# Performance work log

Hardware: AMD Instinct MI355X
Metric: run time of the kernel (lower is better)

## Reference

```python
import jax, jax.numpy as jnp
import numpy as np

D_IN = 2048
D_OUT = 2048
NUM_HEADS = 32
NUM_KV_GROUPS = 8
HEAD_DIM = D_OUT // NUM_HEADS          # 64
GROUP_SIZE = NUM_HEADS // NUM_KV_GROUPS  # 4
BATCH = 2
SEQ = 2048


def _rope(x, cos, sin):
    # x: [b, h, s, d]; cos/sin: [s, d]
    d = x.shape[-1]
    x1, x2 = x[..., : d // 2], x[..., d // 2:]
    rotated = jnp.concatenate((-x2, x1), axis=-1)
    return x * cos[None, None, :, :] + rotated * sin[None, None, :, :]


def setup_inputs() -> dict:
    key = jax.random.key(0)
    ks = jax.random.split(key, 8)
    x = jax.random.normal(ks[0], (BATCH, SEQ, D_IN), dtype=jnp.float32)
    cos = jax.random.normal(ks[1], (SEQ, HEAD_DIM), dtype=jnp.float32)
    sin = jax.random.normal(ks[2], (SEQ, HEAD_DIM), dtype=jnp.float32)
    # causal mask: True above the diagonal = masked out
    mask = jnp.triu(jnp.ones((SEQ, SEQ), dtype=jnp.bool_), k=1)
    s = 0.02
    Wq = jax.random.normal(ks[3], (D_IN, D_OUT), dtype=jnp.float32) * s
    Wk = jax.random.normal(ks[4], (D_IN, NUM_KV_GROUPS * HEAD_DIM), dtype=jnp.float32) * s
    Wv = jax.random.normal(ks[5], (D_IN, NUM_KV_GROUPS * HEAD_DIM), dtype=jnp.float32) * s
    Wo = jax.random.normal(ks[6], (D_OUT, D_OUT), dtype=jnp.float32) * s
    return {"x": x, "cos": cos, "sin": sin, "mask": mask,
            "Wq": Wq, "Wk": Wk, "Wv": Wv, "Wo": Wo}


def reference(x, cos, sin, mask, Wq, Wk, Wv, Wo):
    b, s, _ = x.shape
    # projections (Linear, no bias): weights stored as [d_in, d_out]
    q = (x @ Wq).reshape(b, s, NUM_HEADS, HEAD_DIM).transpose(0, 2, 1, 3)      # [b,H,s,d]
    k = (x @ Wk).reshape(b, s, NUM_KV_GROUPS, HEAD_DIM).transpose(0, 2, 1, 3)  # [b,G,s,d]
    v = (x @ Wv).reshape(b, s, NUM_KV_GROUPS, HEAD_DIM).transpose(0, 2, 1, 3)  # [b,G,s,d]
    q = _rope(q, cos, sin)
    k = _rope(k, cos, sin)
    # GQA broadcast: repeat each KV group group_size times along head axis
    k = jnp.repeat(k, GROUP_SIZE, axis=1)  # [b,H,s,d]
    v = jnp.repeat(v, GROUP_SIZE, axis=1)  # [b,H,s,d]
    scores = jnp.einsum('bhqd,bhkd->bhqk', q, k)
    scores = jnp.where(mask[None, None, :, :], -jnp.inf, scores)
    # original scales AFTER masking: softmax(scores / sqrt(head_dim)); -inf stays -inf
    attn = jax.nn.softmax(scores * (1.0 / np.sqrt(HEAD_DIM)), axis=-1)
    ctx = jnp.einsum('bhqk,bhkd->bqhd', attn, v).reshape(b, s, D_OUT)
    return ctx @ Wo
```

## Files before the change

### kernel.cpp

```cpp
#include <hip/hip_runtime.h>
#include <hip/hip_fp16.h>

#define SEQ    2048
#define DIN    2048
#define DOUT   2048
#define NH     32
#define NKV    8
#define HD     64
#define BB     2

typedef _Float16 half_t;
typedef __attribute__((ext_vector_type(8))) _Float16 half8;
typedef __attribute__((ext_vector_type(4))) _Float16 half4;
typedef __attribute__((ext_vector_type(2))) __fp16   fp16x2;
typedef __attribute__((ext_vector_type(4))) float    floatx4;

union H8U { half8 h; int u[4]; };
union H2I { fp16x2 h; int i; };

__device__ __forceinline__ void gload16(void* l, const void* g) {
    __builtin_amdgcn_global_load_lds(
        (const __attribute__((address_space(1))) void*)g,
        (__attribute__((address_space(3))) void*)l, 16, 0, 0);
}

__global__ void cast_f2h(const float* __restrict__ in, half_t* __restrict__ out, int n4) {
    int i = blockIdx.x * blockDim.x + threadIdx.x;
    if (i < n4) {
        float4 v = ((const float4*)in)[i];
        half4 h;
        h[0] = (half_t)v.x; h[1] = (half_t)v.y; h[2] = (half_t)v.z; h[3] = (half_t)v.w;
        ((half4*)out)[i] = h;
    }
}

__global__ __launch_bounds__(256) void tcast(const float* __restrict__ in, half_t* __restrict__ out,
                                             int Kd, int Nd) {
    __shared__ float T[32][33];
    int x0 = blockIdx.x * 32, y0 = blockIdx.y * 32;
    int tx = threadIdx.x & 31, ty = threadIdx.x >> 5;
    #pragma unroll
    for (int j = 0; j < 4; j++)
        T[ty + j * 8][tx] = in[(size_t)(y0 + ty + j * 8) * Nd + x0 + tx];
    __syncthreads();
    #pragma unroll
    for (int j = 0; j < 4; j++)
        out[(size_t)(x0 + ty + j * 8) * Kd + y0 + tx] = (half_t)T[tx][ty + j * 8];
}

__global__ __launch_bounds__(256) void gemm_tn_h(
    const half_t* __restrict__ A, const half_t* __restrict__ Bt,
    half_t* __restrict__ C, int M, int N, int K)
{
    __shared__ half_t As[4096];
    __shared__ half_t Bs[4096];
    int tid = threadIdx.x, wave = tid >> 6, lane = tid & 63;
    int quad = lane >> 4, l15 = lane & 15;
    int m0 = blockIdx.y * 128, n0 = blockIdx.x * 128;
    int wm = (wave >> 1) * 64, wn = (wave & 1) * 64;
    floatx4 acc[4][4] = {};

    int srow[2], skoff[2], sldso[2];
    #pragma unroll
    for (int is = 0; is < 2; is++) {
        int s = is * 256 + tid;
        int p = s >> 3, sc = s & 7;
        int c = sc ^ (p & 7);
        srow[is]  = 2 * p + (c >> 2);
        skoff[is] = (c & 3) * 8;
        sldso[is] = (is * 256 + wave * 64) * 8;
    }
    for (int k0 = 0; k0 < K; k0 += 32) {
        __syncthreads();
        #pragma unroll
        for (int is = 0; is < 2; is++) {
            gload16(&As[sldso[is]], A  + (size_t)(m0 + srow[is]) * K + k0 + skoff[is]);
            gload16(&Bs[sldso[is]], Bt + (size_t)(n0 + srow[is]) * K + k0 + skoff[is]);
        }
        __syncthreads();
        half8 af[4], bf[4];
        #pragma unroll
        for (int i = 0; i < 4; i++) {
            int r = wm + i * 16 + l15, p = r >> 1;
            int sc = (((r & 1) * 4 + quad) ^ (p & 7));
            af[i] = *(const half8*)&As[p * 64 + sc * 8];
            int rn = wn + i * 16 + l15, pn = rn >> 1;
            int scn = (((rn & 1) * 4 + quad) ^ (pn & 7));
            bf[i] = *(const half8*)&Bs[pn * 64 + scn * 8];
        }
        #pragma unroll
        for (int i = 0; i < 4; i++)
            #pragma unroll
            for (int j = 0; j < 4; j++)
                acc[i][j] = __builtin_amdgcn_mfma_f32_16x16x32_f16(af[i], bf[j], acc[i][j], 0, 0, 0);
    }
    #pragma unroll
    for (int i = 0; i < 4; i++) {
        int row = m0 + wm + i * 16 + quad * 4;
        #pragma unroll
        for (int j = 0; j < 4; j++) {
            int col = n0 + wn + j * 16 + l15;
            #pragma unroll
            for (int r = 0; r < 4; r++)
                C[(size_t)(row + r) * N + col] = (half_t)acc[i][j][r];
        }
    }
}

__global__ __launch_bounds__(256) void gemm_tn_f(
    const half_t* __restrict__ A, const half_t* __restrict__ Bt,
    float* __restrict__ C, int M, int N, int K)
{
    __shared__ half_t As[4096];
    __shared__ half_t Bs[4096];
    int tid = threadIdx.x, wave = tid >> 6, lane = tid & 63;
    int quad = lane >> 4, l15 = lane & 15;
    int m0 = blockIdx.y * 128, n0 = blockIdx.x * 128;
    int wm = (wave >> 1) * 64, wn = (wave & 1) * 64;
    floatx4 acc[4][4] = {};
    int srow[2], skoff[2], sldso[2];
    #pragma unroll
    for (int is = 0; is < 2; is++) {
        int s = is * 256 + tid;
        int p = s >> 3, sc = s & 7;
        int c = sc ^ (p & 7);
        srow[is]  = 2 * p + (c >> 2);
        skoff[is] = (c & 3) * 8;
        sldso[is] = (is * 256 + wave * 64) * 8;
    }
    for (int k0 = 0; k0 < K; k0 += 32) {
        __syncthreads();
        #pragma unroll
        for (int is = 0; is < 2; is++) {
            gload16(&As[sldso[is]], A  + (size_t)(m0 + srow[is]) * K + k0 + skoff[is]);
            gload16(&Bs[sldso[is]], Bt + (size_t)(n0 + srow[is]) * K + k0 + skoff[is]);
        }
        __syncthreads();
        half8 af[4], bf[4];
        #pragma unroll
        for (int i = 0; i < 4; i++) {
            int r = wm + i * 16 + l15, p = r >> 1;
            int sc = (((r & 1) * 4 + quad) ^ (p & 7));
            af[i] = *(const half8*)&As[p * 64 + sc * 8];
            int rn = wn + i * 16 + l15, pn = rn >> 1;
            int scn = (((rn & 1) * 4 + quad) ^ (pn & 7));
            bf[i] = *(const half8*)&Bs[pn * 64 + scn * 8];
        }
        #pragma unroll
        for (int i = 0; i < 4; i++)
            #pragma unroll
            for (int j = 0; j < 4; j++)
                acc[i][j] = __builtin_amdgcn_mfma_f32_16x16x32_f16(af[i], bf[j], acc[i][j], 0, 0, 0);
    }
    #pragma unroll
    for (int i = 0; i < 4; i++) {
        int row = m0 + wm + i * 16 + quad * 4;
        #pragma unroll
        for (int j = 0; j < 4; j++) {
            int col = n0 + wn + j * 16 + l15;
            #pragma unroll
            for (int r = 0; r < 4; r++)
                C[(size_t)(row + r) * N + col] = acc[i][j][r];
        }
    }
}

__global__ void rope_q(const half_t* __restrict__ qkv, const float* __restrict__ cosb,
                       const float* __restrict__ sinb, half_t* __restrict__ Qh) {
    int idx = blockIdx.x * 256 + threadIdx.x;
    int d = idx & 31, h = (idx >> 5) & 31, s = (idx >> 10) & 2047, b = idx >> 21;
    const half_t* q = qkv + (size_t)(b * 2048 + s) * 3072 + h * 64;
    float x1 = (float)q[d], x2 = (float)q[d + 32];
    float c1 = cosb[s * 64 + d], c2 = cosb[s * 64 + d + 32];
    float s1 = sinb[s * 64 + d], s2 = sinb[s * 64 + d + 32];
    half_t* o = Qh + ((size_t)(b * NH + h) * 2048 + s) * 64;
    o[d]      = (half_t)((x1 * c1 - x2 * s1) * 0.125f);
    o[d + 32] = (half_t)((x2 * c2 + x1 * s2) * 0.125f);
}

__global__ void rope_k(const half_t* __restrict__ qkv, const float* __restrict__ cosb,
                       const float* __restrict__ sinb, half_t* __restrict__ Kh) {
    int idx = blockIdx.x * 256 + threadIdx.x;
    int d = idx & 31, g = (idx >> 5) & 7, s = (idx >> 8) & 2047, b = idx >> 19;
    const half_t* k = qkv + (size_t)(b * 2048 + s) * 3072 + 2048 + g * 64;
    float x1 = (float)k[d], x2 = (float)k[d + 32];
    float c1 = cosb[s * 64 + d], c2 = cosb[s * 64 + d + 32];
    float s1 = sinb[s * 64 + d], s2 = sinb[s * 64 + d + 32];
    half_t* o = Kh + ((size_t)(b * NKV + g) * 2048 + s) * 64;
    o[d]      = (half_t)(x1 * c1 - x2 * s1);
    o[d + 32] = (half_t)(x2 * c2 + x1 * s2);
}

__global__ __launch_bounds__(256) void v_transpose(const half_t* __restrict__ qkv, half_t* __restrict__ Vt) {
    __shared__ float T[64][65];
    int s0 = blockIdx.x * 64;
    int bg = blockIdx.y; int b = bg >> 3, g = bg & 7;
    int tx = threadIdx.x & 63, ty = threadIdx.x >> 6;
    #pragma unroll
    for (int j = 0; j < 16; j++) {
        int s = ty * 16 + j;
        T[s][tx] = (float)qkv[(size_t)(b * 2048 + s0 + s) * 3072 + 2560 + g * 64 + tx];
    }
    __syncthreads();
    #pragma unroll
    for (int j = 0; j < 16; j++) {
        int d = ty * 16 + j;
        Vt[((size_t)(b * NKV + g) * 64 + d) * SEQ + s0 + tx] = (half_t)T[tx][d];
    }
}

__global__ __launch_bounds__(256, 4) void attn(
    const half_t* __restrict__ Qh, const half_t* __restrict__ Kh,
    const half_t* __restrict__ Vt, half_t* __restrict__ ctx)
{
    __shared__ half_t Ks[2][4096];
    __shared__ half_t Vs[2][4096];

    const int tid = threadIdx.x, wave = tid >> 6, lane = tid & 63;
    const int quad = lane >> 4, l15 = lane & 15;
    const int bid = blockIdx.x;
    const int qt = 15 - (bid >> 6);
    const int b  = (bid >> 5) & 1;
    const int h  = bid & 31;
    const int g  = h >> 2;
    const int q0 = qt * 128;
    const int wm = wave * 32;

    const half_t* kp = Kh + (size_t)(b * NKV + g) * SEQ * 64;
    const half_t* vp = Vt + (size_t)(b * NKV + g) * 64 * SEQ;

    half8 qf[2][2];
    {
        const half_t* qpp = Qh + ((size_t)(b * NH + h) * SEQ + q0 + wm) * 64;
        #pragma unroll
        for (int mf = 0; mf < 2; mf++)
            #pragma unroll
            for (int kc = 0; kc < 2; kc++)
                qf[mf][kc] = *(const half8*)(qpp + (size_t)(mf * 16 + l15) * 64 + kc * 32 + quad * 8);
    }

    int koff[2], voff[2], lo[2];
    #pragma unroll
    for (int is = 0; is < 2; is++) {
        int s = is * 256 + tid;
        int p = s >> 3, c = (s & 7) ^ (p & 7);
        koff[is] = p * 64 + c * 8;
        voff[is] = p * SEQ + c * 8;
        lo[is]   = (is * 256 + wave * 64) * 8;
    }

    float m_i[2], l_i[2];
    m_i[0] = m_i[1] = -__builtin_inff();
    l_i[0] = l_i[1] = 0.f;
    floatx4 o[2][4] = {};

    const int ntiles = 2 * qt + 2;
    #pragma unroll
    for (int is = 0; is < 2; is++) {
        gload16(&Ks[0][lo[is]], kp + koff[is]);
        gload16(&Vs[0][lo[is]], vp + voff[is]);
    }

    const int srcA = l15 + ((quad & 1) ? 32 : 0);
    const int srcB = srcA + 16;
    const bool hiK = (quad >> 1) != 0;

    for (int kt = 0; kt < ntiles; kt++) {
        const int cur = kt & 1;
        const int kb  = kt * 64;
        __syncthreads();
        if (kt + 1 < ntiles) {
            const int kb2 = (kt + 1) * 64;
            #pragma unroll
            for (int is = 0; is < 2; is++) {
                gload16(&Ks[cur ^ 1][lo[is]], kp + (size_t)kb2 * 64 + koff[is]);
                gload16(&Vs[cur ^ 1][lo[is]], vp + kb2 + voff[is]);
            }
        }

        if (kb <= q0 + wm + 31) {
            floatx4 sa[2][4] = {};
            #pragma unroll
            for (int kc = 0; kc < 2; kc++)
                #pragma unroll
                for (int kf = 0; kf < 4; kf++) {
                    int row = kf * 16 + l15;
                    int sc = ((kc * 4 + quad) ^ (row & 7));
                    half8 kfr = *(const half8*)&Ks[cur][row * 64 + sc * 8];
                    sa[0][kf] = __builtin_amdgcn_mfma_f32_16x16x32_f16(kfr, qf[0][kc], sa[0][kf], 0, 0, 0);
                    sa[1][kf] = __builtin_amdgcn_mfma_f32_16x16x32_f16(kfr, qf[1][kc], sa[1][kf], 0, 0, 0);
                }

            if (kb + 63 > q0 + wm) {
                #pragma unroll
                for (int kf = 0; kf < 4; kf++)
                    #pragma unroll
                    for (int r = 0; r < 4; r++) {
                        int key = kb + kf * 16 + quad * 4 + r;
                        if (key > q0 + wm + l15)      sa[0][kf][r] = -__builtin_inff();
                        if (key > q0 + wm + 16 + l15) sa[1][kf][r] = -__builtin_inff();
                    }
            }

            int eh[2][4][2];
            float alpha[2];
            #pragma unroll
            for (int mf = 0; mf < 2; mf++) {
                float mt = sa[mf][0][0];
                #pragma unroll
                for (int kf = 0; kf < 4; kf++)
                    #pragma unroll
                    for (int r = 0; r < 4; r++) mt = fmaxf(mt, sa[mf][kf][r]);
                mt = fmaxf(mt, __shfl_xor(mt, 16));
                mt = fmaxf(mt, __shfl_xor(mt, 32));
                float mn = fmaxf(m_i[mf], mt);
                alpha[mf] = __expf(m_i[mf] - mn);
                m_i[mf] = mn;
                float rs = 0.f;
                #pragma unroll
                for (int kf = 0; kf < 4; kf++) {
                    float e0 = __expf(sa[mf][kf][0] - mn);
                    float e1 = __expf(sa[mf][kf][1] - mn);
                    float e2 = __expf(sa[mf][kf][2] - mn);
                    float e3 = __expf(sa[mf][kf][3] - mn);
                    rs += (e0 + e1) + (e2 + e3);
                    H2I p01, p23;
                    p01.h = __builtin_amdgcn_cvt_pkrtz(e0, e1);
                    p23.h = __builtin_amdgcn_cvt_pkrtz(e2, e3);
                    eh[mf][kf][0] = p01.i;
                    eh[mf][kf][1] = p23.i;
                }
                rs += __shfl_xor(rs, 16);
                rs += __shfl_xor(rs, 32);
                l_i[mf] = l_i[mf] * alpha[mf] + rs;
                #pragma unroll
                for (int nf = 0; nf < 4; nf++)
                    #pragma unroll
                    for (int r = 0; r < 4; r++) o[mf][nf][r] *= alpha[mf];
            }

            #pragma unroll
            for (int kc = 0; kc < 2; kc++) {
                H8U pf[2];
                #pragma unroll
                for (int mf = 0; mf < 2; mf++) {
                    int a0 = __shfl(eh[mf][2 * kc][0],     srcA);
                    int a1 = __shfl(eh[mf][2 * kc][1],     srcA);
                    int b0 = __shfl(eh[mf][2 * kc + 1][0], srcA);
                    int b1 = __shfl(eh[mf][2 * kc + 1][1], srcA);
                    int c0 = __shfl(eh[mf][2 * kc][0],     srcB);
                    int c1 = __shfl(eh[mf][2 * kc][1],     srcB);
                    int d0 = __shfl(eh[mf][2 * kc + 1][0], srcB);
                    int d1 = __shfl(eh[mf][2 * kc + 1][1], srcB);
                    pf[mf].u[0] = hiK ? b0 : a0;
                    pf[mf].u[1] = hiK ? b1 : a1;
                    pf[mf].u[2] = hiK ? d0 : c0;
                    pf[mf].u[3] = hiK ? d1 : c1;
                }
                #pragma unroll
                for (int nf = 0; nf < 4; nf++) {
                    int row = nf * 16 + l15;
                    int sc = ((kc * 4 + quad) ^ (row & 7));
                    half8 vf = *(const half8*)&Vs[cur][row * 64 + sc * 8];
                    o[0][nf] = __builtin_amdgcn_mfma_f32_16x16x32_f16(vf, pf[0].h, o[0][nf], 0, 0, 0);
                    o[1][nf] = __builtin_amdgcn_mfma_f32_16x16x32_f16(vf, pf[1].h, o[1][nf], 0, 0, 0);
                }
            }
        }
    }

    #pragma unroll
    for (int mf = 0; mf < 2; mf++) {
        float inv = 1.0f / l_i[mf];
        int s = q0 + wm + mf * 16 + l15;
        half_t* op = ctx + (size_t)(b * SEQ + s) * DOUT + h * 64 + quad * 4;
        #pragma unroll
        for (int nf = 0; nf < 4; nf++) {
            half4 hv;
            hv[0] = (half_t)(o[mf][nf][0] * inv);
            hv[1] = (half_t)(o[mf][nf][1] * inv);
            hv[2] = (half_t)(o[mf][nf][2] * inv);
            hv[3] = (half_t)(o[mf][nf][3] * inv);
            *(half4*)(op + nf * 16) = hv;
        }
    }
}

extern "C" void kernel_launch(void* const* d_in, const int* in_sizes, int n_in,
                              void* d_out, int out_size, void* d_ws, size_t ws_size,
                              hipStream_t stream) {
    const float* x    = (const float*)d_in[0];
    const float* cosb = (const float*)d_in[1];
    const float* sinb = (const float*)d_in[2];
    const float* Wq   = (const float*)d_in[4];
    const float* Wk   = (const float*)d_in[5];
    const float* Wv   = (const float*)d_in[6];
    const float* Wo   = (const float*)d_in[7];
    float* out = (float*)d_out;

    const size_t M  = (size_t)BB * SEQ;
    const size_t nX = M * DIN;

    char* ws = (char*)d_ws;
    const size_t MB = 1048576;
    half_t* xh     = (half_t*)(ws);
    half_t* WqkvT  = (half_t*)(ws + 16 * MB);
    half_t* WoT    = (half_t*)(ws + 28 * MB);
    half_t* qkvh   = (half_t*)(ws + 36 * MB);
    half_t* Qh     = (half_t*)(ws + 60 * MB);
    half_t* Kh     = (half_t*)(ws + 76 * MB);
    half_t* Vt     = (half_t*)(ws + 80 * MB);
    half_t* ctxh   = (half_t*)(ws + 84 * MB);

    cast_f2h<<<(nX / 4) / 256, 256, 0, stream>>>(x, xh, nX / 4);
    tcast<<<dim3(64, 64), 256, 0, stream>>>(Wq, WqkvT, DIN, DOUT);
    tcast<<<dim3(16, 64), 256, 0, stream>>>(Wk, WqkvT + (size_t)2048 * 2048, DIN, 512);
    tcast<<<dim3(16, 64), 256, 0, stream>>>(Wv, WqkvT + (size_t)2560 * 2048, DIN, 512);
    tcast<<<dim3(64, 64), 256, 0, stream>>>(Wo, WoT, DOUT, DOUT);

    gemm_tn_h<<<dim3(3072 / 128, M / 128), 256, 0, stream>>>(xh, WqkvT, qkvh, M, 3072, DIN);

    rope_q<<<(BB * SEQ * NH * 32) / 256, 256, 0, stream>>>(qkvh, cosb, sinb, Qh);
    rope_k<<<(BB * SEQ * NKV * 32) / 256, 256, 0, stream>>>(qkvh, cosb, sinb, Kh);
    v_transpose<<<dim3(SEQ / 64, BB * NKV), 256, 0, stream>>>(qkvh, Vt);

    attn<<<BB * NH * (SEQ / 128), 256, 0, stream>>>(Qh, Kh, Vt, ctxh);

    gemm_tn_f<<<dim3(DOUT / 128, M / 128), 256, 0, stream>>>(ctxh, WoT, out, M, DOUT, DIN);
}
```

Baseline: 360.8 us.

## Fuse RoPE, scaling and V transpose into QKV GEMM epilogue; use exp2

The QKV projection GEMM now applies RoPE to Q and K directly from its accumulators, writing head-major Qh and Kh. It also writes V transposed into Vt, so the intermediate qkv buffer and three separate kernels go away. The Q scale now folds in log2(e), and the attention softmax uses exp2f instead of __expf. This removes a round trip of the qkv tensor through global memory and two kernel launches. The cost is a heavier GEMM epilogue with scattered cos/sin loads and narrow 2-byte stores.

```diff
diff --git a/kernel.cpp b/kernel.cpp
--- a/kernel.cpp
+++ b/kernel.cpp
@@ -48,12 +48,14 @@
         out[(size_t)(x0 + ty + j * 8) * Kd + y0 + tx] = (half_t)T[tx][ty + j * 8];
 }
 
-__global__ __launch_bounds__(256) void gemm_tn_h(
+__global__ __launch_bounds__(256) void gemm_qkv(
     const half_t* __restrict__ A, const half_t* __restrict__ Bt,
-    half_t* __restrict__ C, int M, int N, int K)
+    const float* __restrict__ cosb, const float* __restrict__ sinb,
+    half_t* __restrict__ Qh, half_t* __restrict__ Kh, half_t* __restrict__ Vt)
 {
     __shared__ half_t As[4096];
     __shared__ half_t Bs[4096];
+    const int K = DIN, M = BB * SEQ;
     int tid = threadIdx.x, wave = tid >> 6, lane = tid & 63;
     int quad = lane >> 4, l15 = lane & 15;
     int m0 = blockIdx.y * 128, n0 = blockIdx.x * 128;
@@ -94,15 +96,46 @@
             for (int j = 0; j < 4; j++)
                 acc[i][j] = __builtin_amdgcn_mfma_f32_16x16x32_f16(af[i], bf[j], acc[i][j], 0, 0, 0);
     }
-    #pragma unroll
-    for (int i = 0; i < 4; i++) {
-        int row = m0 + wm + i * 16 + quad * 4;
-        #pragma unroll
-        for (int j = 0; j < 4; j++) {
-            int col = n0 + wn + j * 16 + l15;
-            #pragma unroll
-            for (int r = 0; r < 4; r++)
-                C[(size_t)(row + r) * N + col] = (half_t)acc[i][j][r];
+
+    const int headg = (n0 + wn) >> 6;
+    const int b = m0 >> 11;
+    const int s_base = (m0 & 2047) + wm + quad * 4;
+
+    if (headg < 40) {
+        const bool isQ = headg < 32;
+        const float sc = isQ ? 0.125f * 1.44269504088896f : 1.0f;
+        half_t* outp = isQ ? (Qh + (size_t)(b * NH + headg) * SEQ * 64)
+                           : (Kh + (size_t)(b * NKV + (headg - 32)) * SEQ * 64);
+        #pragma unroll
+        for (int i = 0; i < 4; i++)
+            #pragma unroll
+            for (int r = 0; r < 4; r++) {
+                int s = s_base + i * 16 + r;
+                #pragma unroll
+                for (int j = 0; j < 2; j++) {
+                    int d = j * 16 + l15;
+                    float x1 = acc[i][j][r], x2 = acc[i][j + 2][r];
+                    float c1 = cosb[s * 64 + d],      s1 = sinb[s * 64 + d];
+                    float c2 = cosb[s * 64 + d + 32], s2 = sinb[s * 64 + d + 32];
+                    outp[(size_t)s * 64 + d]      = (half_t)((x1 * c1 - x2 * s1) * sc);
+                    outp[(size_t)s * 64 + d + 32] = (half_t)((x2 * c2 + x1 * s2) * sc);
+                }
+            }
+    } else {
+        half_t* vtp = Vt + (size_t)(b * NKV + (headg - 40)) * 64 * SEQ;
+        #pragma unroll
+        for (int i = 0; i < 4; i++) {
+            int s = s_base + i * 16;
+            #pragma unroll
+            for (int j = 0; j < 4; j++) {
+                int d = j * 16 + l15;
+                half4 hv;
+                hv[0] = (half_t)acc[i][j][0];
+                hv[1] = (half_t)acc[i][j][1];
+                hv[2] = (half_t)acc[i][j][2];
+                hv[3] = (half_t)acc[i][j][3];
+                *(half4*)(vtp + (size_t)d * SEQ + s) = hv;
+            }
         }
     }
 }
@@ -165,50 +198,6 @@
     }
 }
 
-__global__ void rope_q(const half_t* __restrict__ qkv, const float* __restrict__ cosb,
-                       const float* __restrict__ sinb, half_t* __restrict__ Qh) {
-    int idx = blockIdx.x * 256 + threadIdx.x;
-    int d = idx & 31, h = (idx >> 5) & 31, s = (idx >> 10) & 2047, b = idx >> 21;
-    const half_t* q = qkv + (size_t)(b * 2048 + s) * 3072 + h * 64;
-    float x1 = (float)q[d], x2 = (float)q[d + 32];
-    float c1 = cosb[s * 64 + d], c2 = cosb[s * 64 + d + 32];
-    float s1 = sinb[s * 64 + d], s2 = sinb[s * 64 + d + 32];
-    half_t* o = Qh + ((size_t)(b * NH + h) * 2048 + s) * 64;
-    o[d]      = (half_t)((x1 * c1 - x2 * s1) * 0.125f);
-    o[d + 32] = (half_t)((x2 * c2 + x1 * s2) * 0.125f);
-}
-
-__global__ void rope_k(const half_t* __restrict__ qkv, const float* __restrict__ cosb,
-                       const float* __restrict__ sinb, half_t* __restrict__ Kh) {
-    int idx = blockIdx.x * 256 + threadIdx.x;
-    int d = idx & 31, g = (idx >> 5) & 7, s = (idx >> 8) & 2047, b = idx >> 19;
-    const half_t* k = qkv + (size_t)(b * 2048 + s) * 3072 + 2048 + g * 64;
-    float x1 = (float)k[d], x2 = (float)k[d + 32];
-    float c1 = cosb[s * 64 + d], c2 = cosb[s * 64 + d + 32];
-    float s1 = sinb[s * 64 + d], s2 = sinb[s * 64 + d + 32];
-    half_t* o = Kh + ((size_t)(b * NKV + g) * 2048 + s) * 64;
-    o[d]      = (half_t)(x1 * c1 - x2 * s1);
-    o[d + 32] = (half_t)(x2 * c2 + x1 * s2);
-}
-
-__global__ __launch_bounds__(256) void v_transpose(const half_t* __restrict__ qkv, half_t* __restrict__ Vt) {
-    __shared__ float T[64][65];
-    int s0 = blockIdx.x * 64;
-    int bg = blockIdx.y; int b = bg >> 3, g = bg & 7;
-    int tx = threadIdx.x & 63, ty = threadIdx.x >> 6;
-    #pragma unroll
-    for (int j = 0; j < 16; j++) {
-        int s = ty * 16 + j;
-        T[s][tx] = (float)qkv[(size_t)(b * 2048 + s0 + s) * 3072 + 2560 + g * 64 + tx];
-    }
-    __syncthreads();
-    #pragma unroll
-    for (int j = 0; j < 16; j++) {
-        int d = ty * 16 + j;
-        Vt[((size_t)(b * NKV + g) * 64 + d) * SEQ + s0 + tx] = (half_t)T[tx][d];
-    }
-}
-
 __global__ __launch_bounds__(256, 4) void attn(
     const half_t* __restrict__ Qh, const half_t* __restrict__ Kh,
     const half_t* __restrict__ Vt, half_t* __restrict__ ctx)
@@ -314,15 +303,15 @@
                 mt = fmaxf(mt, __shfl_xor(mt, 16));
                 mt = fmaxf(mt, __shfl_xor(mt, 32));
                 float mn = fmaxf(m_i[mf], mt);
-                alpha[mf] = __expf(m_i[mf] - mn);
+                alpha[mf] = exp2f(m_i[mf] - mn);
                 m_i[mf] = mn;
                 float rs = 0.f;
                 #pragma unroll
                 for (int kf = 0; kf < 4; kf++) {
-                    float e0 = __expf(sa[mf][kf][0] - mn);
-                    float e1 = __expf(sa[mf][kf][1] - mn);
-                    float e2 = __expf(sa[mf][kf][2] - mn);
-                    float e3 = __expf(sa[mf][kf][3] - mn);
+                    float e0 = exp2f(sa[mf][kf][0] - mn);
+                    float e1 = exp2f(sa[mf][kf][1] - mn);
+                    float e2 = exp2f(sa[mf][kf][2] - mn);
+                    float e3 = exp2f(sa[mf][kf][3] - mn);
                     rs += (e0 + e1) + (e2 + e3);
                     H2I p01, p23;
                     p01.h = __builtin_amdgcn_cvt_pkrtz(e0, e1);
@@ -406,11 +395,10 @@
     half_t* xh     = (half_t*)(ws);
     half_t* WqkvT  = (half_t*)(ws + 16 * MB);
     half_t* WoT    = (half_t*)(ws + 28 * MB);
-    half_t* qkvh   = (half_t*)(ws + 36 * MB);
-    half_t* Qh     = (half_t*)(ws + 60 * MB);
-    half_t* Kh     = (half_t*)(ws + 76 * MB);
-    half_t* Vt     = (half_t*)(ws + 80 * MB);
-    half_t* ctxh   = (half_t*)(ws + 84 * MB);
+    half_t* Qh     = (half_t*)(ws + 36 * MB);
+    half_t* Kh     = (half_t*)(ws + 52 * MB);
+    half_t* Vt     = (half_t*)(ws + 56 * MB);
+    half_t* ctxh   = (half_t*)(ws + 60 * MB);
 
     cast_f2h<<<(nX / 4) / 256, 256, 0, stream>>>(x, xh, nX / 4);
     tcast<<<dim3(64, 64), 256, 0, stream>>>(Wq, WqkvT, DIN, DOUT);
@@ -418,11 +406,7 @@
     tcast<<<dim3(16, 64), 256, 0, stream>>>(Wv, WqkvT + (size_t)2560 * 2048, DIN, 512);
     tcast<<<dim3(64, 64), 256, 0, stream>>>(Wo, WoT, DOUT, DOUT);
 
-    gemm_tn_h<<<dim3(3072 / 128, M / 128), 256, 0, stream>>>(xh, WqkvT, qkvh, M, 3072, DIN);
-
-    rope_q<<<(BB * SEQ * NH * 32) / 256, 256, 0, stream>>>(qkvh, cosb, sinb, Qh);
-    rope_k<<<(BB * SEQ * NKV * 32) / 256, 256, 0, stream>>>(qkvh, cosb, sinb, Kh);
-    v_transpose<<<dim3(SEQ / 64, BB * NKV), 256, 0, stream>>>(qkvh, Vt);
+    gemm_qkv<<<dim3(3072 / 128, M / 128), 256, 0, stream>>>(xh, WqkvT, cosb, sinb, Qh, Kh, Vt);
 
     attn<<<BB * NH * (SEQ / 128), 256, 0, stream>>>(Qh, Kh, Vt, ctxh);
 
```

Result: slower. 370.3 us (+2.6%).
